# Kernel optimization log

Hardware: AMD Instinct MI355X
Metric: run time of the kernel (lower is better)

The kernel has to match this reference:

```python
import jax, jax.numpy as jnp
import numpy as np

# Architecture constants (from init_kwargs / mamba_ssm Mamba2 defaults)
D_MODEL = 256
D_STATE = 64
D_CONV = 4
EXPAND = 2
HEADDIM = 64
D_INNER = EXPAND * D_MODEL          # 512
NHEADS = D_INNER // HEADDIM         # 8
CONV_DIM = D_INNER + 2 * D_STATE    # 640 (ngroups=1)
D_IN_PROJ = 2 * D_INNER + 2 * D_STATE + NHEADS  # 1160
NUM_LAYERS = 4
EPS = 1e-5


def _mamba2_block(h, ipw, cw, cb, dtb, alog, dpar, rmsw, opw):
    # h: (b, l, d_model)
    b, l, _ = h.shape
    zxbcdt = h @ ipw                                  # (b, l, D_IN_PROJ)
    z = zxbcdt[..., :D_INNER]
    xBC = zxbcdt[..., D_INNER:D_INNER + CONV_DIM]
    dt = zxbcdt[..., -NHEADS:]

    # causal depthwise conv1d over the sequence, then SiLU
    xBC = jnp.swapaxes(xBC, 1, 2)                     # (b, CONV_DIM, l)
    xBC = jax.lax.conv_general_dilated(
        xBC, cw[:, None, :], (1,), [(D_CONV - 1, 0)],
        feature_group_count=CONV_DIM)
    xBC = jax.nn.silu(xBC + cb[None, :, None])
    xBC = jnp.swapaxes(xBC, 1, 2)                     # (b, l, CONV_DIM)

    xh = xBC[..., :D_INNER].reshape(b, l, NHEADS, HEADDIM)
    Bm = xBC[..., D_INNER:D_INNER + D_STATE]          # (b, l, n)
    Cm = xBC[..., D_INNER + D_STATE:]                 # (b, l, n)

    dt = jax.nn.softplus(dt + dtb)                    # (b, l, h)
    A = -jnp.exp(alog)                                # (h,)

    def step(state, ins):
        # state: (b, h, p, n)
        x_t, dt_t, B_t, C_t = ins                     # (b,h,p),(b,h),(b,n),(b,n)
        dA = jnp.exp(dt_t * A)                        # (b, h)
        state = state * dA[:, :, None, None] + jnp.einsum('bh,bhp,bn->bhpn', dt_t, x_t, B_t)
        y = jnp.einsum('bhpn,bn->bhp', state, C_t)
        return state, y

    xs = (jnp.swapaxes(xh, 0, 1), jnp.swapaxes(dt, 0, 1),
          jnp.swapaxes(Bm, 0, 1), jnp.swapaxes(Cm, 0, 1))
    init = jnp.zeros((b, NHEADS, HEADDIM, D_STATE), h.dtype)
    _, ys = jax.lax.scan(step, init, xs)              # ys: (l, b, h, p)
    y = jnp.swapaxes(ys, 0, 1) + dpar[None, None, :, None] * xh
    y = y.reshape(b, l, D_INNER)

    # gated RMSNorm (norm(y * silu(z)) * weight), then out projection
    y = y * jax.nn.silu(z)
    y = y * jax.lax.rsqrt(jnp.mean(y * y, -1, keepdims=True) + EPS) * rmsw
    return y @ opw


def setup_inputs() -> dict:
    key = jax.random.key(0)
    ks = jax.random.split(key, 12)
    B, L, F = 16, 2048, 46
    inp = {
        'x': jax.random.normal(ks[0], (B, L, F), jnp.float32),
        'inp_w': jax.random.normal(ks[1], (F, D_MODEL), jnp.float32) * 0.1,
        'inp_b': jnp.zeros((D_MODEL,), jnp.float32),
        'in_proj_w': jax.random.normal(ks[2], (NUM_LAYERS, D_MODEL, D_IN_PROJ), jnp.float32) * 0.02,
        'conv_w': jax.random.normal(ks[3], (NUM_LAYERS, CONV_DIM, D_CONV), jnp.float32) * 0.2,
        'conv_b': jnp.zeros((NUM_LAYERS, CONV_DIM), jnp.float32),
        'dt_bias': jax.random.normal(ks[4], (NUM_LAYERS, NHEADS), jnp.float32) * 0.5,
        'A_log': jnp.log(jax.random.uniform(ks[5], (NUM_LAYERS, NHEADS), jnp.float32, 1.0, 16.0)),
        'D': jnp.ones((NUM_LAYERS, NHEADS), jnp.float32),
        'rms_w': jnp.ones((NUM_LAYERS, D_INNER), jnp.float32),
        'out_proj_w': jax.random.normal(ks[6], (NUM_LAYERS, D_INNER, D_MODEL), jnp.float32) * 0.02,
        'ln_w': jnp.ones((D_MODEL,), jnp.float32),
        'ln_b': jnp.zeros((D_MODEL,), jnp.float32),
        'dir_w': jax.random.normal(ks[7], (D_MODEL, 1), jnp.float32) * 0.05,
        'dir_b': jnp.zeros((1,), jnp.float32),
        'reg_w': jax.random.normal(ks[8], (D_MODEL, 3), jnp.float32) * 0.05,
        'reg_b': jnp.zeros((3,), jnp.float32),
    }
    return inp


def reference(x, inp_w, inp_b, in_proj_w, conv_w, conv_b, dt_bias, A_log, D,
              rms_w, out_proj_w, ln_w, ln_b, dir_w, dir_b, reg_w, reg_b):
    h = x @ inp_w + inp_b
    for i in range(NUM_LAYERS):
        h = h + _mamba2_block(h, in_proj_w[i], conv_w[i], conv_b[i], dt_bias[i],
                              A_log[i], D[i], rms_w[i], out_proj_w[i])
    mu = jnp.mean(h, -1, keepdims=True)
    var = jnp.mean((h - mu) ** 2, -1, keepdims=True)
    h = (h - mu) * jax.lax.rsqrt(var + EPS) * ln_w + ln_b
    h = jnp.mean(h, axis=1)                           # mean-pool over sequence
    # dropout is identity in eval mode
    dir_logits = h @ dir_w + dir_b
    reg_out = h @ reg_w + reg_b
    return (dir_logits, reg_out)
```

## Files before the change

### kernel.cpp

```cpp
#include <hip/hip_runtime.h>
#include <hip/hip_bf16.h>
#include <math.h>

typedef __hip_bfloat16 bf16;

#define B_ 16
#define L_ 2048
#define DM 256
#define DI 512
#define NH 8
#define HD 64
#define DS 64
#define CD 640
#define DIP 1160
#define XB 648
#define NP 1280
#define NL 4
#define Q_ 64
#define NCH 32
#define MROWS (B_*L_)
#define EPS_ 1e-5f
#define NIN 17
#define NSMALL 14
#define STGOFF 32
#define WIPT 28552
#define WOPT 683912
#define HMPOFF 946056
#define SLICEOFF 1011592
#define PERROW 2004

__device__ __forceinline__ float u2f(unsigned short u){ return __uint_as_float(((unsigned)u)<<16); }
__device__ __forceinline__ unsigned short f2bu(float f){ bf16 h = __float2bfloat16(f); return *(unsigned short*)&h; }
__device__ __forceinline__ float sigmoidf_(float x){ return 1.f/(1.f+__expf(-x)); }
__device__ __forceinline__ float siluf_(float x){ return x*sigmoidf_(x); }
__device__ __forceinline__ float softplusf_(float x){ return (x>20.f)? x : log1pf(__expf(x)); }

typedef __attribute__((ext_vector_type(8))) short short8v;
typedef __attribute__((ext_vector_type(4))) float float4v;

__device__ const int kN17[NIN] = {1507328,11776,256,1187840,10240,2560,32,32,32,2048,524288,256,256,256,1,768,3};
__device__ const int sIdx[NSMALL] = {1,2,4,5,6,7,8,9,11,12,13,14,15,16};
__device__ const int sNum[NSMALL] = {11776,256,10240,2560,32,32,32,2048,256,256,256,1,768,3};
__device__ const int sOff[NSMALL] = {0,11776,12032,22272,24832,24864,24896,24928,26976,27232,27488,27744,27748,28516};

struct PtrTab { const void* p[NIN]; };

__global__ __launch_bounds__(64) void k_sentinel(float* out, float v){
    int t = threadIdx.x;
    out[t] = (t==0) ? v : 0.f;
}

__global__ __launch_bounds__(256) void k_detect(PtrTab t, int* flags){
    int i = blockIdx.x;
    int n = kN17[i];
    int S = n < 4096 ? n : 4096;
    const unsigned short* u = (const unsigned short*)t.p[i];
    __shared__ int big, ze, zo, so;
    if (threadIdx.x == 0){ big=0; ze=0; zo=0; so=0; }
    __syncthreads();
    int lbig=0, lze=0, lzo=0, lso=0;
    for (int j=threadIdx.x; j<S; j+=256){
        unsigned short v = u[j];
        int e = (v>>7)&0xFF;
        if (e >= 131) lbig = 1;
        int isz = ((v & 0x7FFF) == 0) ? 1 : 0;
        if (j & 1){ lso++; lzo += isz; } else { lze += isz; }
    }
    if (lbig) atomicOr(&big, 1);
    atomicAdd(&ze, lze); atomicAdd(&zo, lzo); atomicAdd(&so, lso);
    __syncthreads();
    if (threadIdx.x == 0){
        int Se = S - so;
        flags[i] = (big || (so > 0 && 4*ze >= 3*Se && 4*zo <= so)) ? 1 : 0;
    }
}

__global__ __launch_bounds__(256) void k_stage(PtrTab t, const int* __restrict__ flags,
                                               float* __restrict__ stg){
    int a = blockIdx.y;
    int idx = sIdx[a];
    int n = sNum[a];
    float* dst = stg + sOff[a];
    const void* p = t.p[idx];
    if (flags[idx]){
        const float* s = (const float*)p;
        for (int j=blockIdx.x*256+threadIdx.x; j<n; j += gridDim.x*256) dst[j] = s[j];
    } else {
        const unsigned short* s = (const unsigned short*)p;
        for (int j=blockIdx.x*256+threadIdx.x; j<n; j += gridDim.x*256) dst[j] = u2f(s[j]);
    }
}

__global__ __launch_bounds__(256) void k_wip(const void* __restrict__ src,
                                             const int* __restrict__ flag,
                                             unsigned short* __restrict__ dst){
    int n = blockIdx.x, l = blockIdx.y, k = threadIdx.x;
    unsigned short b = 0;
    if (n < DIP){
        size_t si = ((size_t)l*DM + k)*DIP + n;
        if (flag[0]) b = f2bu(((const float*)src)[si]);
        else         b = ((const unsigned short*)src)[si];
    }
    dst[((size_t)l*NP + n)*DM + k] = b;
}

__global__ __launch_bounds__(256) void k_wop(const void* __restrict__ src,
                                             const int* __restrict__ flag,
                                             unsigned short* __restrict__ dst){
    int n = blockIdx.x, l = blockIdx.y;
    for (int k = threadIdx.x; k < DI; k += 256){
        size_t si = ((size_t)l*DI + k)*DM + n;
        unsigned short b;
        if (flag[0]) b = f2bu(((const float*)src)[si]);
        else         b = ((const unsigned short*)src)[si];
        dst[((size_t)l*DM + n)*DI + k] = b;
    }
}

__device__ __forceinline__ float blockSum256(float v, float* red){
    #pragma unroll
    for (int off=32; off>0; off>>=1) v += __shfl_down(v, off);
    if ((threadIdx.x & 63) == 0) red[threadIdx.x >> 6] = v;
    __syncthreads();
    float s = red[0] + red[1] + red[2] + red[3];
    __syncthreads();
    return s;
}

__global__ __launch_bounds__(256) void k_inproj(const void* __restrict__ x,
                                                const int* __restrict__ flags,
                                                size_t xoff,
                                                const float* __restrict__ w,
                                                const float* __restrict__ bias,
                                                float* __restrict__ h,
                                                unsigned short* __restrict__ hbf){
    __shared__ float xs[32*46];
    int row0 = blockIdx.x*32;
    int t = threadIdx.x;
    bool f32 = flags[0] != 0;
    for (int j = t; j < 32*46; j += 256){
        size_t gi = xoff + (size_t)row0*46 + j;
        xs[j] = f32 ? ((const float*)x)[gi] : u2f(((const unsigned short*)x)[gi]);
    }
    __syncthreads();
    float bv = bias[t];
    float acc[32];
    #pragma unroll
    for (int r=0;r<32;r++) acc[r] = bv;
    for (int k=0;k<46;k++){
        float wv = w[k*DM + t];
        #pragma unroll
        for (int r=0;r<32;r++) acc[r] += xs[r*46 + k]*wv;
    }
    #pragma unroll
    for (int r=0;r<32;r++){
        size_t o = (size_t)(row0 + r)*DM + t;
        h[o] = acc[r];
        hbf[o] = f2bu(acc[r]);
    }
}

template<int MODE>
__global__ __launch_bounds__(256) void k_mgemm(const unsigned short* __restrict__ A,
                                               const unsigned short* __restrict__ Bt,
                                               float* __restrict__ O1,
                                               unsigned short* __restrict__ O1b,
                                               unsigned short* __restrict__ O2b,
                                               unsigned short* __restrict__ O3,
                                               int K){
    __shared__ unsigned short As[128*40];
    __shared__ unsigned short Bs[128*40];
    int tid = threadIdx.x;
    int wave = tid >> 6, lane = tid & 63, quad = lane >> 4, l15 = lane & 15;
    int p = blockIdx.y * gridDim.x + blockIdx.x;
    int nwg = gridDim.x * gridDim.y;
    int cpx = nwg >> 3;
    int logical = (p & 7) * cpx + (p >> 3);
    int by = logical / gridDim.x;
    int bx = logical - by * gridDim.x;
    int mbase = by*128, nbase = bx*128;
    int wm = (wave & 1)*64, wn = (wave >> 1)*64;
    float4v zero4 = {0.f,0.f,0.f,0.f};
    float4v acc[4][4];
    #pragma unroll
    for (int mi=0;mi<4;mi++)
        #pragma unroll
        for (int ni=0;ni<4;ni++) acc[mi][ni] = zero4;
    for (int k0 = 0; k0 < K; k0 += 32){
        #pragma unroll
        for (int i=0;i<2;i++){
            int c = tid + i*256;
            int row = c >> 2, koff = (c & 3)*8;
            *(uint4*)&As[row*40 + koff] = *(const uint4*)&A[(size_t)(mbase+row)*K + k0 + koff];
            *(uint4*)&Bs[row*40 + koff] = *(const uint4*)&Bt[(size_t)(nbase+row)*K + k0 + koff];
        }
        __syncthreads();
        short8v af[4], bfr[4];
        #pragma unroll
        for (int mi=0;mi<4;mi++) af[mi] = *(const short8v*)&As[(wm + mi*16 + l15)*40 + quad*8];
        #pragma unroll
        for (int ni=0;ni<4;ni++) bfr[ni] = *(const short8v*)&Bs[(wn + ni*16 + l15)*40 + quad*8];
        #pragma unroll
        for (int mi=0;mi<4;mi++)
            #pragma unroll
            for (int ni=0;ni<4;ni++)
                acc[mi][ni] = __builtin_amdgcn_mfma_f32_16x16x32_bf16(af[mi], bfr[ni], acc[mi][ni], 0, 0, 0);
        __syncthreads();
    }
    #pragma unroll
    for (int mi=0;mi<4;mi++){
        #pragma unroll
        for (int ni=0;ni<4;ni++){
            int col = nbase + wn + ni*16 + l15;
            #pragma unroll
            for (int reg=0;reg<4;reg++){
                int grow = mbase + wm + mi*16 + quad*4 + reg;
                float v = acc[mi][ni][reg];
                if (MODE == 0){
                    if (col < DI) O1b[(size_t)grow*DI + col] = f2bu(v);
                    else if (col < DIP) O2b[(size_t)grow*XB + (col - DI)] = f2bu(v);
                } else {
                    float hnew = O1[(size_t)grow*DM + col] + v;
                    O1[(size_t)grow*DM + col] = hnew;
                    O3[(size_t)grow*DM + col] = f2bu(hnew);
                }
            }
        }
    }
}

__global__ __launch_bounds__(256) void k_conv(const unsigned short* __restrict__ xbb,
                                              const float* __restrict__ cw,
                                              const float* __restrict__ cb,
                                              unsigned short* __restrict__ cvb){
    int tid = threadIdx.x;
    int c0 = (blockIdx.x*16 + (tid & 15))*4;
    int r0 = blockIdx.y*64 + (tid >> 4);
    float wA[4], wB[4], wC[4], wD[4];
    {
        float4 t0 = *(const float4*)&cw[(size_t)(c0+0)*4];
        float4 t1 = *(const float4*)&cw[(size_t)(c0+1)*4];
        float4 t2 = *(const float4*)&cw[(size_t)(c0+2)*4];
        float4 t3 = *(const float4*)&cw[(size_t)(c0+3)*4];
        wA[0]=t0.x; wA[1]=t0.y; wA[2]=t0.z; wA[3]=t0.w;
        wB[0]=t1.x; wB[1]=t1.y; wB[2]=t1.z; wB[3]=t1.w;
        wC[0]=t2.x; wC[1]=t2.y; wC[2]=t2.z; wC[3]=t2.w;
        wD[0]=t3.x; wD[1]=t3.y; wD[2]=t3.z; wD[3]=t3.w;
    }
    float4 bb = *(const float4*)&cb[c0];
    #pragma unroll
    for (int i=0;i<4;i++){
        int r = r0 + i*16;
        int l = r & (L_-1);
        float a0=bb.x, a1=bb.y, a2=bb.z, a3=bb.w;
        #pragma unroll
        for (int j=0;j<4;j++){
            if (l-3+j >= 0){
                ushort4 uv = *(const ushort4*)&xbb[(size_t)(r-3+j)*XB + c0];
                a0 += u2f(uv.x)*wA[j];
                a1 += u2f(uv.y)*wB[j];
                a2 += u2f(uv.z)*wC[j];
                a3 += u2f(uv.w)*wD[j];
            }
        }
        ushort4 ov;
        ov.x = f2bu(siluf_(a0));
        ov.y = f2bu(siluf_(a1));
        ov.z = f2bu(siluf_(a2));
        ov.w = f2bu(siluf_(a3));
        *(ushort4*)&cvb[(size_t)r*CD + c0] = ov;
    }
}

__global__ __launch_bounds__(64) void k_dtcum(const unsigned short* __restrict__ xb,
                                              const float* __restrict__ dtb,
                                              const float* __restrict__ alog,
                                              float* __restrict__ dto,
                                              float* __restrict__ cumo){
    int kk = blockIdx.x, h = blockIdx.y, b = blockIdx.z;
    int t = threadIdx.x;
    int l = kk*Q_ + t;
    float raw = u2f(xb[(size_t)(b*L_ + l)*XB + CD + h]);
    float dtv = softplusf_(raw + dtb[h]);
    float A = -__expf(alog[h]);
    float s = dtv * A;
    #pragma unroll
    for (int off=1; off<64; off<<=1){
        float u = __shfl_up(s, off);
        if (t >= off) s += u;
    }
    int base = (b*NH + h)*L_ + l;
    dto[base] = dtv;
    cumo[base] = s;
}

__device__ __forceinline__ void grp_map(int p, int &kk, int &h, int &b){
    int c = p & 7, i = p >> 3;
    h = i & 7;
    int g = (i & ~7) | c;
    kk = g & (NCH-1);
    b = g >> 5;
}

__global__ __launch_bounds__(256) void k_passS(const unsigned short* __restrict__ cvb,
                                               const float* __restrict__ dt,
                                               const float* __restrict__ cum,
                                               float* __restrict__ S){
    __shared__ unsigned short Bw[64*72];
    __shared__ unsigned short Xt[64*72];
    __shared__ float sw[64];
    int kk, h, b;
    grp_map(blockIdx.x, kk, h, b);
    int tid = threadIdx.x;
    int bh = b*NH + h;
    int l0 = kk*Q_;
    if (tid < 64){
        int base = bh*L_ + l0;
        float c = cum[base + tid];
        float c63 = cum[base + 63];
        sw[tid] = dt[base + tid]*__expf(fminf(c63 - c, 0.f));
    }
    __syncthreads();
    int srow = tid >> 4, c0 = (tid & 15)*4;
    #pragma unroll
    for (int i=0;i<4;i++){
        int s = srow + i*16;
        size_t rb = ((size_t)(b*L_ + l0 + s))*CD;
        ushort4 bv = *(const ushort4*)&cvb[rb + DI + c0];
        ushort4 xv = *(const ushort4*)&cvb[rb + h*HD + c0];
        float w = sw[s];
        Bw[(c0+0)*72 + s] = f2bu(w*u2f(bv.x));
        Bw[(c0+1)*72 + s] = f2bu(w*u2f(bv.y));
        Bw[(c0+2)*72 + s] = f2bu(w*u2f(bv.z));
        Bw[(c0+3)*72 + s] = f2bu(w*u2f(bv.w));
        Xt[(c0+0)*72 + s] = xv.x;
        Xt[(c0+1)*72 + s] = xv.y;
        Xt[(c0+2)*72 + s] = xv.z;
        Xt[(c0+3)*72 + s] = xv.w;
    }
    __syncthreads();
    int wave = tid >> 6, lane = tid & 63, quad = lane >> 4, l15 = lane & 15;
    int wn = (wave & 1)*32, wp = (wave >> 1)*32;
    float4v zero4 = {0.f,0.f,0.f,0.f};
    float4v acc[2][2];
    #pragma unroll
    for (int mi=0;mi<2;mi++)
        #pragma unroll
        for (int ni=0;ni<2;ni++) acc[mi][ni] = zero4;
    #pragma unroll
    for (int k0=0;k0<64;k0+=32){
        short8v af[2], bfr[2];
        #pragma unroll
        for (int mi=0;mi<2;mi++) af[mi] = *(const short8v*)&Bw[(wn + mi*16 + l15)*72 + k0 + quad*8];
        #pragma unroll
        for (int ni=0;ni<2;ni++) bfr[ni] = *(const short8v*)&Xt[(wp + ni*16 + l15)*72 + k0 + quad*8];
        #pragma unroll
        for (int mi=0;mi<2;mi++)
            #pragma unroll
            for (int ni=0;ni<2;ni++)
                acc[mi][ni] = __builtin_amdgcn_mfma_f32_16x16x32_bf16(af[mi], bfr[ni], acc[mi][ni], 0, 0, 0);
    }
    size_t Sbase = ((size_t)bh*NCH + kk)*4096;
    #pragma unroll
    for (int mi=0;mi<2;mi++){
        #pragma unroll
        for (int ni=0;ni<2;ni++){
            int p = wp + ni*16 + l15;
            #pragma unroll
            for (int reg=0;reg<4;reg++){
                int n = wn + mi*16 + quad*4 + reg;
                S[Sbase + n*64 + p] = acc[mi][ni][reg];
            }
        }
    }
}

__global__ __launch_bounds__(256) void k_combine(const float* __restrict__ cum,
                                                 float* __restrict__ S){
    int h = blockIdx.x, b = blockIdx.y, z = blockIdx.z;
    int bh = b*NH + h;
    int tid = threadIdx.x;
    float4 st = make_float4(0.f,0.f,0.f,0.f);
    size_t base0 = ((size_t)bh*NCH)*4096 + (size_t)z*1024 + (size_t)tid*4;
    for (int k=0;k<NCH;k++){
        size_t base = base0 + (size_t)k*4096;
        float dk = __expf(fminf(cum[bh*L_ + k*Q_ + 63], 0.f));
        float4 a = *(const float4*)&S[base];
        *(float4*)&S[base] = st;
        st.x = a.x + dk*st.x;
        st.y = a.y + dk*st.y;
        st.z = a.z + dk*st.z;
        st.w = a.w + dk*st.w;
    }
}

__global__ __launch_bounds__(256) void k_finalize2(const unsigned short* __restrict__ cvb,
                                                   const float* __restrict__ dt,
                                                   const float* __restrict__ cum,
                                                   const float* __restrict__ Dp,
                                                   const float* __restrict__ S,
                                                   unsigned short* __restrict__ yB){
    __shared__ unsigned short Ct[64*72];
    __shared__ unsigned short Bs[64*72];
    __shared__ unsigned short Xt[64*72];
    __shared__ unsigned short St[64*72];
    __shared__ float sdt[64], scum[64];
    unsigned short* const Ml = &Bs[0];
    int kk, h, b;
    grp_map(blockIdx.x, kk, h, b);
    int tid = threadIdx.x;
    int bh = b*NH + h;
    int l0 = kk*Q_;
    if (tid < 64){
        int base = bh*L_ + l0;
        sdt[tid] = dt[base + tid];
        scum[tid] = cum[base + tid];
    }
    int rr = tid >> 4, c0 = (tid & 15)*4;
    size_t Sbase = ((size_t)bh*NCH + kk)*4096;
    #pragma unroll
    for (int i=0;i<4;i++){
        int r = rr + i*16;
        size_t rb = ((size_t)(b*L_ + l0 + r))*CD;
        *(ushort4*)&Ct[r*72 + c0] = *(const ushort4*)&cvb[rb + DI + DS + c0];
        *(ushort4*)&Bs[r*72 + c0] = *(const ushort4*)&cvb[rb + DI + c0];
        ushort4 xv = *(const ushort4*)&cvb[rb + h*HD + c0];
        Xt[(c0+0)*72 + r] = xv.x;
        Xt[(c0+1)*72 + r] = xv.y;
        Xt[(c0+2)*72 + r] = xv.z;
        Xt[(c0+3)*72 + r] = xv.w;
        float4 sv = *(const float4*)&S[Sbase + r*64 + c0];
        St[(c0+0)*72 + r] = f2bu(sv.x);
        St[(c0+1)*72 + r] = f2bu(sv.y);
        St[(c0+2)*72 + r] = f2bu(sv.z);
        St[(c0+3)*72 + r] = f2bu(sv.w);
    }
    __syncthreads();
    int wave = tid >> 6, lane = tid & 63, quad = lane >> 4, l15 = lane & 15;
    int wt2 = (wave & 1)*32, wc = (wave >> 1)*32;
    float4v zero4 = {0.f,0.f,0.f,0.f};
    {
        float4v acc[2][2];
        #pragma unroll
        for (int mi=0;mi<2;mi++)
            #pragma unroll
            for (int ni=0;ni<2;ni++) acc[mi][ni] = zero4;
        #pragma unroll
        for (int k0=0;k0<64;k0+=32){
            short8v af[2], bfr[2];
            #pragma unroll
            for (int mi=0;mi<2;mi++) af[mi] = *(const short8v*)&Ct[(wt2 + mi*16 + l15)*72 + k0 + quad*8];
            #pragma unroll
            for (int ni=0;ni<2;ni++) bfr[ni] = *(const short8v*)&Bs[(wc + ni*16 + l15)*72 + k0 + quad*8];
            #pragma unroll
            for (int mi=0;mi<2;mi++)
                #pragma unroll
                for (int ni=0;ni<2;ni++)
                    acc[mi][ni] = __builtin_amdgcn_mfma_f32_16x16x32_bf16(af[mi], bfr[ni], acc[mi][ni], 0, 0, 0);
        }
        __syncthreads();
        #pragma unroll
        for (int mi=0;mi<2;mi++){
            #pragma unroll
            for (int ni=0;ni<2;ni++){
                int s = wc + ni*16 + l15;
                #pragma unroll
                for (int reg=0;reg<4;reg++){
                    int t = wt2 + mi*16 + quad*4 + reg;
                    float m = (s <= t) ? acc[mi][ni][reg]*sdt[s]*__expf(fminf(scum[t]-scum[s], 0.f)) : 0.f;
                    Ml[t*72 + s] = f2bu(m);
                }
            }
        }
    }
    __syncthreads();
    {
        float4v a1[2][2], a2[2][2];
        #pragma unroll
        for (int mi=0;mi<2;mi++)
            #pragma unroll
            for (int ni=0;ni<2;ni++){ a1[mi][ni] = zero4; a2[mi][ni] = zero4; }
        #pragma unroll
        for (int k0=0;k0<64;k0+=32){
            short8v mf[2], cf[2], xf[2], sf[2];
            #pragma unroll
            for (int mi=0;mi<2;mi++){
                mf[mi] = *(const short8v*)&Ml[(wt2 + mi*16 + l15)*72 + k0 + quad*8];
                cf[mi] = *(const short8v*)&Ct[(wt2 + mi*16 + l15)*72 + k0 + quad*8];
            }
            #pragma unroll
            for (int ni=0;ni<2;ni++){
                xf[ni] = *(const short8v*)&Xt[(wc + ni*16 + l15)*72 + k0 + quad*8];
                sf[ni] = *(const short8v*)&St[(wc + ni*16 + l15)*72 + k0 + quad*8];
            }
            #pragma unroll
            for (int mi=0;mi<2;mi++)
                #pragma unroll
                for (int ni=0;ni<2;ni++){
                    a1[mi][ni] = __builtin_amdgcn_mfma_f32_16x16x32_bf16(mf[mi], xf[ni], a1[mi][ni], 0, 0, 0);
                    a2[mi][ni] = __builtin_amdgcn_mfma_f32_16x16x32_bf16(cf[mi], sf[ni], a2[mi][ni], 0, 0, 0);
                }
        }
        float Dh = Dp[h];
        #pragma unroll
        for (int mi=0;mi<2;mi++){
            #pragma unroll
            for (int ni=0;ni<2;ni++){
                int p = wc + ni*16 + l15;
                #pragma unroll
                for (int reg=0;reg<4;reg++){
                    int t = wt2 + mi*16 + quad*4 + reg;
                    float e = __expf(fminf(scum[t], 0.f));
                    float xval = u2f(Xt[p*72 + t]);
                    yB[(size_t)(b*L_ + l0 + t)*DI + h*HD + p] =
                        f2bu(a1[mi][ni][reg] + e*a2[mi][ni][reg] + Dh*xval);
                }
            }
        }
    }
}

__global__ __launch_bounds__(256) void k_gaterms(const unsigned short* __restrict__ z,
                                                 const float* __restrict__ rw,
                                                 const unsigned short* __restrict__ yB,
                                                 unsigned short* __restrict__ ybf){
    __shared__ float red[4];
    int row = blockIdx.x;
    int tid = threadIdx.x;
    float g[2]; float ss = 0.f;
    #pragma unroll
    for (int r=0;r<2;r++){
        int d = tid + r*256;
        float zv = u2f(z[(size_t)row*DI + d]);
        float yv = u2f(yB[(size_t)row*DI + d]);
        float gv = yv * siluf_(zv);
        g[r] = gv;
        ss += gv*gv;
    }
    float tot = blockSum256(ss, red);
    float rinv = rsqrtf(tot*(1.f/512.f) + EPS_);
    #pragma unroll
    for (int r=0;r<2;r++){
        int d = tid + r*256;
        ybf[(size_t)row*DI + d] = f2bu(g[r]*rinv*rw[d]);
    }
}

__global__ __launch_bounds__(256) void k_ln(const float* __restrict__ h,
                                            const float* __restrict__ lw,
                                            const float* __restrict__ lb,
                                            float* __restrict__ out){
    __shared__ float red[4];
    int row = blockIdx.x;
    int tid = threadIdx.x;
    float v = h[(size_t)row*DM + tid];
    float mu = blockSum256(v, red)*(1.f/256.f);
    float d = v - mu;
    float var = blockSum256(d*d, red)*(1.f/256.f);
    out[(size_t)row*DM + tid] = d*rsqrtf(var + EPS_)*lw[tid] + lb[tid];
}

__global__ __launch_bounds__(256) void k_meanl(const float* __restrict__ ln,
                                               float* __restrict__ hmp,
                                               int b0){
    int g = blockIdx.x, bl = blockIdx.y;
    int tid = threadIdx.x;
    float s = 0.f;
    for (int i=0;i<128;i++){
        int l = g*128 + i;
        s += ln[(size_t)(bl*L_ + l)*DM + tid];
    }
    hmp[((size_t)(b0+bl)*16 + g)*DM + tid] = s*(1.f/2048.f);
}

__global__ __launch_bounds__(256) void k_heads(const float* __restrict__ hmp,
                                               const float* __restrict__ dw,
                                               const float* __restrict__ db,
                                               const float* __restrict__ rw,
                                               const float* __restrict__ rb,
                                               float* __restrict__ out){
    __shared__ float red[4];
    int b = blockIdx.x;
    int tid = threadIdx.x;
    float hv = 0.f;
    #pragma unroll
    for (int g=0; g<16; g++) hv += hmp[((size_t)b*16 + g)*DM + tid];
    float s0 = hv*dw[tid];
    float s1 = hv*rw[tid*3+0];
    float s2 = hv*rw[tid*3+1];
    float s3 = hv*rw[tid*3+2];
    s0 = blockSum256(s0, red);
    s1 = blockSum256(s1, red);
    s2 = blockSum256(s2, red);
    s3 = blockSum256(s3, red);
    if (tid == 0){
        out[b] = s0 + db[0];
        out[16 + b*3 + 0] = s1 + rb[0];
        out[16 + b*3 + 1] = s2 + rb[1];
        out[16 + b*3 + 2] = s3 + rb[2];
    }
}

extern "C" void kernel_launch(void* const* d_in, const int* in_sizes, int n_in,
                              void* d_out, int out_size, void* d_ws, size_t ws_size,
                              hipStream_t stream){
    static const int expSizes[NIN] = {1507328,11776,256,1187840,10240,2560,32,32,32,2048,524288,256,256,256,1,768,3};
    float* out = (float*)d_out;

    if (n_in != NIN){
        k_sentinel<<<1,64,0,stream>>>(out, 9.0e6f);
        return;
    }
    for (int i=0;i<NIN;i++){
        if (in_sizes[i] != expSizes[i]){
            k_sentinel<<<1,64,0,stream>>>(out, (float)(i+1)*1.0e5f);
            return;
        }
    }
    size_t need16 = ((size_t)SLICEOFF + 2048ull*PERROW)*4ull;
    if (ws_size < need16){
        float mb = (float)(ws_size >> 20);
        k_sentinel<<<1,64,0,stream>>>(out, 2.0e7f + mb*131072.f);
        return;
    }

    float* ws = (float*)d_ws;
    int* flags = (int*)d_ws;
    float* stg = ws + STGOFF;
    unsigned short* ipwT = (unsigned short*)(ws + WIPT);
    unsigned short* opwT = (unsigned short*)(ws + WOPT);
    float* hmp = ws + HMPOFF;

    PtrTab pt;
    for (int i=0;i<NIN;i++) pt.p[i] = d_in[i];

    k_detect<<<NIN, 256, 0, stream>>>(pt, flags);
    k_stage<<<dim3(8, NSMALL), 256, 0, stream>>>(pt, flags, stg);
    k_wip<<<dim3(NP, NL), 256, 0, stream>>>(d_in[3], flags+3, ipwT);
    k_wop<<<dim3(DM, NL), 256, 0, stream>>>(d_in[10], flags+10, opwT);

    const float* inp_w = stg + 0;
    const float* inp_b = stg + 11776;
    const float* cw    = stg + 12032;
    const float* cb    = stg + 22272;
    const float* dtb   = stg + 24832;
    const float* alog  = stg + 24864;
    const float* Dp    = stg + 24896;
    const float* rmsw  = stg + 24928;
    const float* lnw   = stg + 26976;
    const float* lnb   = stg + 27232;
    const float* dw    = stg + 27488;
    const float* db    = stg + 27744;
    const float* rw    = stg + 27748;
    const float* rb    = stg + 28516;

    int nsl = 1;
    while (((size_t)SLICEOFF + ((size_t)MROWS/nsl)*PERROW)*4ull > ws_size) nsl <<= 1;
    const size_t R = (size_t)MROWS / nsl;
    const int SB = B_ / nsl;

    float* base = ws + SLICEOFF;
    float* hbuf = base;
    unsigned short* hbf  = (unsigned short*)(base + R*256);
    unsigned short* zb   = (unsigned short*)(base + R*384);
    unsigned short* xbb  = (unsigned short*)(base + R*640);
    unsigned short* ybB  = (unsigned short*)(base + R*640);
    unsigned short* cvb  = (unsigned short*)(base + R*964);
    unsigned short* ybf  = (unsigned short*)(base + R*964);
    float* S   = base + R*1284;
    float* dt  = base + R*1796;
    float* cum = base + R*1804;

    for (int sl=0; sl<nsl; sl++){
        k_inproj<<<(int)(R/32), 256, 0, stream>>>(d_in[0], flags, (size_t)sl*R*46, inp_w, inp_b, hbuf, hbf);
        for (int li=0; li<NL; li++){
            const float* cwl = cw + li*CD*4;
            const float* cbl = cb + li*CD;
            k_mgemm<0><<<dim3(NP/128, R/128), 256, 0, stream>>>(
                hbf, ipwT + (size_t)li*NP*DM, hbuf, zb, xbb, ybf, DM);
            k_conv<<<dim3(10, (int)(R/64)), 256, 0, stream>>>(xbb, cwl, cbl, cvb);
            k_dtcum<<<dim3(NCH,NH,SB), 64, 0, stream>>>(xbb, dtb + li*NH, alog + li*NH, dt, cum);
            k_passS<<<NCH*NH*SB, 256, 0, stream>>>(cvb, dt, cum, S);
            k_combine<<<dim3(NH,SB,4), 256, 0, stream>>>(cum, S);
            k_finalize2<<<NCH*NH*SB, 256, 0, stream>>>(cvb, dt, cum, Dp + li*NH, S, ybB);
            k_gaterms<<<(int)R, 256, 0, stream>>>(zb, rmsw + li*DI, ybB, ybf);
            k_mgemm<1><<<dim3(DM/128, R/128), 256, 0, stream>>>(
                ybf, opwT + (size_t)li*DM*DI, hbuf, zb, xbb, hbf, DI);
        }
        k_ln<<<(int)R, 256, 0, stream>>>(hbuf, lnw, lnb, S);
        k_meanl<<<dim3(16,SB), 256, 0, stream>>>(S, hmp, sl*SB);
    }
    k_heads<<<B_, 256, 0, stream>>>(hmp, dw, db, rw, rb, out);
}
```

Before: 1.051 ms.

## Double-buffer GEMM tiles with direct global-to-LDS async loads

Replaces the register-staged global loads in the MFMA GEMM with global_load_lds instructions that write 16-byte chunks straight into LDS. It double-buffers the A and B tiles so the next K-slice is fetched while MFMAs run on the current one. The LDS layout becomes k-chunk-major with no padding, which changes the fragment read addressing. The intent is to hide global load latency and drop a barrier per iteration. The risks are LDS bank conflicts in the new layout and the lack of an explicit vmcnt wait before the barrier that guards the async writes.

```diff
diff --git a/kernel.cpp b/kernel.cpp
--- a/kernel.cpp
+++ b/kernel.cpp
@@ -38,6 +38,13 @@
 typedef __attribute__((ext_vector_type(8))) short short8v;
 typedef __attribute__((ext_vector_type(4))) float float4v;
 
+__device__ __forceinline__ void gl_lds16(const unsigned short* g, unsigned short* l){
+    __builtin_amdgcn_global_load_lds(
+        (const __attribute__((address_space(1))) unsigned int*)g,
+        (__attribute__((address_space(3))) unsigned int*)l,
+        16, 0, 0);
+}
+
 __device__ const int kN17[NIN] = {1507328,11776,256,1187840,10240,2560,32,32,32,2048,524288,256,256,256,1,768,3};
 __device__ const int sIdx[NSMALL] = {1,2,4,5,6,7,8,9,11,12,13,14,15,16};
 __device__ const int sNum[NSMALL] = {11776,256,10240,2560,32,32,32,2048,256,256,256,1,768,3};
@@ -168,8 +175,8 @@
                                                unsigned short* __restrict__ O2b,
                                                unsigned short* __restrict__ O3,
                                                int K){
-    __shared__ unsigned short As[128*40];
-    __shared__ unsigned short Bs[128*40];
+    __shared__ unsigned short As[2][4096];
+    __shared__ unsigned short Bs[2][4096];
     int tid = threadIdx.x;
     int wave = tid >> 6, lane = tid & 63, quad = lane >> 4, l15 = lane & 15;
     int p = blockIdx.y * gridDim.x + blockIdx.x;
@@ -186,26 +193,45 @@
     for (int mi=0;mi<4;mi++)
         #pragma unroll
         for (int ni=0;ni<4;ni++) acc[mi][ni] = zero4;
-    for (int k0 = 0; k0 < K; k0 += 32){
-        #pragma unroll
-        for (int i=0;i<2;i++){
-            int c = tid + i*256;
-            int row = c >> 2, koff = (c & 3)*8;
-            *(uint4*)&As[row*40 + koff] = *(const uint4*)&A[(size_t)(mbase+row)*K + k0 + koff];
-            *(uint4*)&Bs[row*40 + koff] = *(const uint4*)&Bt[(size_t)(nbase+row)*K + k0 + koff];
-        }
-        __syncthreads();
+
+    int nt = K >> 5;
+    int lbase0 = (wave*64)*8;
+    int lbase1 = (256 + wave*64)*8;
+    int row0 = tid & 127, kc0 = tid >> 7;
+    int row1 = row0, kc1 = kc0 + 2;
+    const unsigned short* Arow0 = A + (size_t)(mbase+row0)*K;
+    const unsigned short* Brow0 = Bt + (size_t)(nbase+row0)*K;
+
+    gl_lds16(Arow0 + kc0*8, &As[0][lbase0]);
+    gl_lds16(Brow0 + kc0*8, &Bs[0][lbase0]);
+    gl_lds16(Arow0 + kc1*8, &As[0][lbase1]);
+    gl_lds16(Brow0 + kc1*8, &Bs[0][lbase1]);
+    __syncthreads();
+
+    int cur = 0;
+    for (int t = 0; t < nt; ++t){
+        if (t+1 < nt){
+            int nb = cur ^ 1;
+            int ko = (t+1)*32;
+            gl_lds16(Arow0 + ko + kc0*8, &As[nb][lbase0]);
+            gl_lds16(Brow0 + ko + kc0*8, &Bs[nb][lbase0]);
+            gl_lds16(Arow0 + ko + kc1*8, &As[nb][lbase1]);
+            gl_lds16(Brow0 + ko + kc1*8, &Bs[nb][lbase1]);
+        }
+        const unsigned short* Ac = &As[cur][0];
+        const unsigned short* Bc = &Bs[cur][0];
         short8v af[4], bfr[4];
         #pragma unroll
-        for (int mi=0;mi<4;mi++) af[mi] = *(const short8v*)&As[(wm + mi*16 + l15)*40 + quad*8];
-        #pragma unroll
-        for (int ni=0;ni<4;ni++) bfr[ni] = *(const short8v*)&Bs[(wn + ni*16 + l15)*40 + quad*8];
+        for (int mi=0;mi<4;mi++) af[mi] = *(const short8v*)&Ac[(quad*128 + wm + mi*16 + l15)*8];
+        #pragma unroll
+        for (int ni=0;ni<4;ni++) bfr[ni] = *(const short8v*)&Bc[(quad*128 + wn + ni*16 + l15)*8];
         #pragma unroll
         for (int mi=0;mi<4;mi++)
             #pragma unroll
             for (int ni=0;ni<4;ni++)
                 acc[mi][ni] = __builtin_amdgcn_mfma_f32_16x16x32_bf16(af[mi], bfr[ni], acc[mi][ni], 0, 0, 0);
         __syncthreads();
+        cur ^= 1;
     }
     #pragma unroll
     for (int mi=0;mi<4;mi++){
```

Result: slower. 1.102 ms (+4.8%).
